# Optimization experiments

Measured on AMD Instinct MI355X. Metric: run time of the kernel, lower is better.

The kernel has to match this reference:

```python
import jax, jax.numpy as jnp
import numpy as np

B, T, D, H, F = 4, 2048, 1024, 16, 4096
HD = D // H
EPS = 1e-5


def setup_inputs() -> dict:
    key = jax.random.key(0)
    ks = jax.random.split(key, 10)
    s = lambda fan_in: 1.0 / np.sqrt(fan_in)
    return {
        "x": jax.random.normal(ks[0], (B, T, D), jnp.float32),
        "ln1_g": jnp.ones((D,), jnp.float32),
        "ln1_b": jnp.zeros((D,), jnp.float32),
        "ln2_g": jnp.ones((D,), jnp.float32),
        "ln2_b": jnp.zeros((D,), jnp.float32),
        "Wq": jax.random.normal(ks[1], (H, D, HD), jnp.float32) * s(D),
        "Wk": jax.random.normal(ks[2], (H, D, HD), jnp.float32) * s(D),
        "Wv": jax.random.normal(ks[3], (H, D, HD), jnp.float32) * s(D),
        "Wo": jax.random.normal(ks[4], (D, D), jnp.float32) * s(D),
        "bo": jnp.zeros((D,), jnp.float32),
        "W1": jax.random.normal(ks[5], (D, F), jnp.float32) * s(D),
        "b1": jnp.zeros((F,), jnp.float32),
        "W2": jax.random.normal(ks[6], (F, D), jnp.float32) * s(F),
        "b2": jnp.zeros((D,), jnp.float32),
    }


def _layernorm(x, g, b):
    mu = jnp.mean(x, axis=-1, keepdims=True)
    var = jnp.mean(jnp.square(x - mu), axis=-1, keepdims=True)
    return (x - mu) * jax.lax.rsqrt(var + EPS) * g + b


def reference(x, ln1_g, ln1_b, ln2_g, ln2_b, Wq, Wk, Wv, Wo, bo, W1, b1, W2, b2):
    Bc, Tc, Dc = x.shape
    xn = _layernorm(x, ln1_g, ln1_b)
    # per-head projections (source loops over heads; here batched over h)
    q = jnp.einsum('btd,hdk->bhtk', xn, Wq)
    k = jnp.einsum('btd,hdk->bhtk', xn, Wk)
    v = jnp.einsum('btd,hdk->bhtk', xn, Wv)
    scale = jnp.asarray(Dc, x.dtype) ** -0.5  # C**-0.5 with C = embedding_dim
    scores = jnp.einsum('bhtk,bhsk->bhts', q, k) * scale
    causal = jnp.tril(jnp.ones((Tc, Tc), bool))
    scores = jnp.where(causal, scores, -jnp.inf)
    attn = jax.nn.softmax(scores, axis=-1)
    out = jnp.einsum('bhts,bhsk->bhtk', attn, v)
    out = out.transpose(0, 2, 1, 3).reshape(Bc, Tc, Dc)  # concat heads
    attn_out = out @ Wo + bo
    h = attn_out + x  # residual 1
    hn = _layernorm(h, ln2_g, ln2_b)
    ff = jax.nn.relu(hn @ W1 + b1) @ W2 + b2
    return ff + h  # residual 2
```

## Files before the change

kernel.cpp:

```cpp
#include <hip/hip_runtime.h>
#include <hip/hip_bf16.h>

#define NB 4
#define NT 2048
#define ND 1024
#define NH 16
#define NHD 64
#define NF 4096
#define MTOK (NB*NT)

typedef float f32x4 __attribute__((ext_vector_type(4)));
typedef __bf16 bf16x8 __attribute__((ext_vector_type(8)));
typedef short s16x8 __attribute__((ext_vector_type(8)));
typedef unsigned short ushort_t;

__device__ inline ushort_t f2bf(float f) {
    unsigned int u = __builtin_bit_cast(unsigned int, f);
    unsigned int r = (u + 0x7FFFu + ((u >> 16) & 1u)) >> 16;
    return (ushort_t)r;
}
__device__ inline float bf2f(ushort_t u) {
    return __builtin_bit_cast(float, (unsigned int)u << 16);
}

__device__ __forceinline__ void async_load16(const void* g, void* l) {
    __builtin_amdgcn_global_load_lds(
        (const __attribute__((address_space(1))) void*)g,
        (__attribute__((address_space(3))) void*)l, 16, 0, 0);
}

__device__ __forceinline__ unsigned int cvt_pk_bf16(float lo, float hi) {
    unsigned int r;
    asm("v_cvt_pk_bf16_f32 %0, %1, %2" : "=v"(r) : "v"(lo), "v"(hi));
    return r;
}

__device__ __forceinline__ float exp2_fast(float x) {
    float r;
    asm("v_exp_f32 %0, %1" : "=v"(r) : "v"(x));
    return r;
}

__global__ __launch_bounds__(256)
void transpose_to_bf16(const float* __restrict__ src, ushort_t* __restrict__ dst,
                       int R, int C) {
    __shared__ float tile[32][33];
    int c0 = blockIdx.x * 32, r0 = blockIdx.y * 32;
    #pragma unroll
    for (int i = 0; i < 32; i += 8)
        tile[threadIdx.y + i][threadIdx.x] =
            src[(size_t)(r0 + threadIdx.y + i) * C + c0 + threadIdx.x];
    __syncthreads();
    #pragma unroll
    for (int i = 0; i < 32; i += 8)
        dst[(size_t)(c0 + threadIdx.y + i) * R + r0 + threadIdx.x] =
            f2bf(tile[threadIdx.x][threadIdx.y + i]);
}

__global__ __launch_bounds__(256)
void transpose_qkv_to_bf16(const float* __restrict__ Wq, const float* __restrict__ Wk,
                           const float* __restrict__ Wv, ushort_t* __restrict__ dst) {
    __shared__ float tile[32][33];
    int z = blockIdx.z;
    int w = z >> 4, h = z & 15;
    const float* src = (w == 0 ? Wq : (w == 1 ? Wk : Wv)) + (size_t)h * ND * NHD;
    const float sc = (w == 0) ? 0.03125f * 1.44269504f : 1.0f;
    ushort_t* out = dst + ((size_t)w * ND + h * NHD) * ND;
    int c0 = blockIdx.x * 32, r0 = blockIdx.y * 32;
    #pragma unroll
    for (int i = 0; i < 32; i += 8)
        tile[threadIdx.y + i][threadIdx.x] =
            src[(size_t)(r0 + threadIdx.y + i) * NHD + c0 + threadIdx.x];
    __syncthreads();
    #pragma unroll
    for (int i = 0; i < 32; i += 8)
        out[(size_t)(c0 + threadIdx.y + i) * ND + r0 + threadIdx.x] =
            f2bf(tile[threadIdx.x][threadIdx.y + i] * sc);
}

__global__ __launch_bounds__(256)
void layernorm_to_bf16(const float* __restrict__ x, const float* __restrict__ g,
                       const float* __restrict__ bvec, ushort_t* __restrict__ out) {
    int row = blockIdx.x;
    const float4* xr = (const float4*)(x + (size_t)row * ND);
    float4 v = xr[threadIdx.x];
    float s = v.x + v.y + v.z + v.w;
    float s2 = v.x * v.x + v.y * v.y + v.z * v.z + v.w * v.w;
    #pragma unroll
    for (int o = 32; o >= 1; o >>= 1) {
        s += __shfl_xor(s, o);
        s2 += __shfl_xor(s2, o);
    }
    __shared__ float red[8];
    int wave = threadIdx.x >> 6, lane = threadIdx.x & 63;
    if (lane == 0) { red[wave] = s; red[4 + wave] = s2; }
    __syncthreads();
    float ts = red[0] + red[1] + red[2] + red[3];
    float ts2 = red[4] + red[5] + red[6] + red[7];
    float mu = ts * (1.f / ND);
    float var = ts2 * (1.f / ND) - mu * mu;
    float rs = rsqrtf(var + 1e-5f);
    float4 gv = ((const float4*)g)[threadIdx.x];
    float4 bv = ((const float4*)bvec)[threadIdx.x];
    ushort4 o4;
    o4.x = f2bf((v.x - mu) * rs * gv.x + bv.x);
    o4.y = f2bf((v.y - mu) * rs * gv.y + bv.y);
    o4.z = f2bf((v.z - mu) * rs * gv.z + bv.z);
    o4.w = f2bf((v.w - mu) * rs * gv.w + bv.w);
    ((ushort4*)(out + (size_t)row * ND))[threadIdx.x] = o4;
}

__global__ __launch_bounds__(256)
void layernorm_bf16(const ushort_t* __restrict__ x, const float* __restrict__ g,
                    const float* __restrict__ bvec, ushort_t* __restrict__ out) {
    int row = blockIdx.x;
    ushort4 u4 = ((const ushort4*)(x + (size_t)row * ND))[threadIdx.x];
    float4 v;
    v.x = bf2f(u4.x); v.y = bf2f(u4.y); v.z = bf2f(u4.z); v.w = bf2f(u4.w);
    float s = v.x + v.y + v.z + v.w;
    float s2 = v.x * v.x + v.y * v.y + v.z * v.z + v.w * v.w;
    #pragma unroll
    for (int o = 32; o >= 1; o >>= 1) {
        s += __shfl_xor(s, o);
        s2 += __shfl_xor(s2, o);
    }
    __shared__ float red[8];
    int wave = threadIdx.x >> 6, lane = threadIdx.x & 63;
    if (lane == 0) { red[wave] = s; red[4 + wave] = s2; }
    __syncthreads();
    float ts = red[0] + red[1] + red[2] + red[3];
    float ts2 = red[4] + red[5] + red[6] + red[7];
    float mu = ts * (1.f / ND);
    float var = ts2 * (1.f / ND) - mu * mu;
    float rs = rsqrtf(var + 1e-5f);
    float4 gv = ((const float4*)g)[threadIdx.x];
    float4 bv = ((const float4*)bvec)[threadIdx.x];
    ushort4 o4;
    o4.x = f2bf((v.x - mu) * rs * gv.x + bv.x);
    o4.y = f2bf((v.y - mu) * rs * gv.y + bv.y);
    o4.z = f2bf((v.z - mu) * rs * gv.z + bv.z);
    o4.w = f2bf((v.w - mu) * rs * gv.w + bv.w);
    ((ushort4*)(out + (size_t)row * ND))[threadIdx.x] = o4;
}

template<int BN, bool HAS_BIAS, bool RELU, int RES_MODE, bool OUT_F32>
__global__ __launch_bounds__(512, 2)
void gemm8p(const ushort_t* __restrict__ A, const ushort_t* __restrict__ Bt,
            const float* __restrict__ bias, const void* __restrict__ res,
            void* __restrict__ outp, int M, int N, int K) {
    constexpr int NFR = BN / 64;
    __shared__ __align__(16) ushort_t As[2][256 * 64];
    __shared__ __align__(16) ushort_t Bs[2][BN * 64];
    const int t = threadIdx.x;
    const int wave = t >> 6, lane = t & 63;
    const int wm = wave >> 2, wn = wave & 3;
    const int g = lane >> 4, l16 = lane & 15;
    int wid = blockIdx.y * gridDim.x + blockIdx.x;
    const int cpx = (gridDim.x * gridDim.y) >> 3;
    wid = (wid & 7) * cpx + (wid >> 3);
    const int m0 = (wid / gridDim.x) * 256;
    const int n0 = (wid % gridDim.x) * BN;
    const int lrow8 = lane >> 3;
    const int srcCol = ((lane & 7) ^ lrow8) * 8;
    const ushort_t* Abase = A + (size_t)m0 * K + srcCol;
    const ushort_t* Bbase = Bt + (size_t)n0 * K + srcCol;
    const int NKT = K >> 6;

    f32x4 acc[8][NFR] = {};

    auto stageAhalf = [&](int kt, int h, int slot) {
        #pragma unroll
        for (int j = 2 * h; j < 2 * h + 2; j++) {
            const int rowbase = j * 64 + wave * 8;
            async_load16(Abase + (size_t)(rowbase + lrow8) * K + kt * 64,
                         &As[slot][rowbase * 64]);
        }
    };
    auto stageBhalf = [&](int kt, int h, int slot) {
        if constexpr (BN == 256) {
            #pragma unroll
            for (int j = 2 * h; j < 2 * h + 2; j++) {
                const int rowbase = j * 64 + wave * 8;
                async_load16(Bbase + (size_t)(rowbase + lrow8) * K + kt * 64,
                             &Bs[slot][rowbase * 64]);
            }
        } else {
            const int rowbase = h * 64 + wave * 8;
            async_load16(Bbase + (size_t)(rowbase + lrow8) * K + kt * 64,
                         &Bs[slot][rowbase * 64]);
        }
    };

    stageAhalf(0, 0, 0); stageAhalf(0, 1, 0);
    stageBhalf(0, 0, 0); stageBhalf(0, 1, 0);
    stageBhalf(1, 0, 1); stageBhalf(1, 1, 1);
    stageAhalf(1, 0, 1);
    if constexpr (BN == 256) asm volatile("s_waitcnt vmcnt(6)" ::: "memory");
    else                     asm volatile("s_waitcnt vmcnt(4)" ::: "memory");
    __builtin_amdgcn_s_barrier();
    __builtin_amdgcn_sched_barrier(0);

    for (int kt = 0; kt < NKT; ++kt) {
        const int cur = kt & 1, nxt = cur ^ 1;
        const ushort_t* as = As[cur];
        const ushort_t* bs = Bs[cur];
        bf16x8 bfr[NFR][2];

        if constexpr (BN == 128) {
            #pragma unroll
            for (int ph = 0; ph < 2; ph++) {
                if (ph == 0) {
                    #pragma unroll
                    for (int nf = 0; nf < NFR; nf++)
                        #pragma unroll
                        for (int ks = 0; ks < 2; ks++) {
                            const int row = wn * (BN / 4) + nf * 16 + l16;
                            int a = row * 128 + ks * 64 + 16 * g;
                            a ^= (row & 7) << 4;
                            bfr[nf][ks] = *(const bf16x8*)((const char*)bs + a);
                        }
                }
                bf16x8 af[2][2][2];
                #pragma unroll
                for (int qq = 0; qq < 2; qq++)
                    #pragma unroll
                    for (int mi2 = 0; mi2 < 2; mi2++)
                        #pragma unroll
                        for (int ks = 0; ks < 2; ks++) {
                            const int row = (ph * 2 + qq) * 64 + wm * 32 + mi2 * 16 + l16;
                            int a = row * 128 + ks * 64 + 16 * g;
                            a ^= (row & 7) << 4;
                            af[qq][mi2][ks] = *(const bf16x8*)((const char*)as + a);
                        }
                if (ph == 0) {
                    if (kt + 1 < NKT) stageAhalf(kt + 1, 1, nxt);
                } else {
                    if (kt + 2 < NKT) {
                        stageBhalf(kt + 2, 0, cur);
                        stageBhalf(kt + 2, 1, cur);
                        stageAhalf(kt + 2, 0, cur);
                    }
                }
                __builtin_amdgcn_sched_barrier(0);
                if (ph == 1) {
                    if (kt >= NKT - 2) asm volatile("s_waitcnt vmcnt(0)" ::: "memory");
                    else               asm volatile("s_waitcnt vmcnt(4)" ::: "memory");
                }
                __builtin_amdgcn_s_barrier();
                __builtin_amdgcn_sched_barrier(0);
                __builtin_amdgcn_s_setprio(1);
                #pragma unroll
                for (int qq = 0; qq < 2; qq++)
                    #pragma unroll
                    for (int mi2 = 0; mi2 < 2; mi2++)
                        #pragma unroll
                        for (int nf = 0; nf < NFR; nf++)
                            #pragma unroll
                            for (int ks = 0; ks < 2; ks++)
                                acc[(ph * 2 + qq) * 2 + mi2][nf] =
                                    __builtin_amdgcn_mfma_f32_16x16x32_bf16(
                                        af[qq][mi2][ks], bfr[nf][ks],
                                        acc[(ph * 2 + qq) * 2 + mi2][nf], 0, 0, 0);
                __builtin_amdgcn_s_setprio(0);
                __builtin_amdgcn_s_barrier();
                __builtin_amdgcn_sched_barrier(0);
            }
        } else {
            #pragma unroll
            for (int q = 0; q < 4; q++) {
                if (q == 0) {
                    #pragma unroll
                    for (int nf = 0; nf < NFR; nf++)
                        #pragma unroll
                        for (int ks = 0; ks < 2; ks++) {
                            const int row = wn * (BN / 4) + nf * 16 + l16;
                            int a = row * 128 + ks * 64 + 16 * g;
                            a ^= (row & 7) << 4;
                            bfr[nf][ks] = *(const bf16x8*)((const char*)bs + a);
                        }
                }
                bf16x8 af[2][2];
                #pragma unroll
                for (int mi2 = 0; mi2 < 2; mi2++)
                    #pragma unroll
                    for (int ks = 0; ks < 2; ks++) {
                        const int row = q * 64 + wm * 32 + mi2 * 16 + l16;
                        int a = row * 128 + ks * 64 + 16 * g;
                        a ^= (row & 7) << 4;
                        af[mi2][ks] = *(const bf16x8*)((const char*)as + a);
                    }
                if (q == 0)      { if (kt + 1 < NKT) stageAhalf(kt + 1, 1, nxt); }
                else if (q == 1) { if (kt + 2 < NKT) stageBhalf(kt + 2, 0, cur); }
                else if (q == 2) { if (kt + 2 < NKT) stageBhalf(kt + 2, 1, cur); }
                else             { if (kt + 2 < NKT) stageAhalf(kt + 2, 0, cur); }
                __builtin_amdgcn_sched_barrier(0);
                if (q == 3) {
                    if (kt >= NKT - 2) asm volatile("s_waitcnt vmcnt(0)" ::: "memory");
                    else               asm volatile("s_waitcnt vmcnt(6)" ::: "memory");
                }
                __builtin_amdgcn_s_barrier();
                __builtin_amdgcn_sched_barrier(0);
                __builtin_amdgcn_s_setprio(1);
                #pragma unroll
                for (int mi2 = 0; mi2 < 2; mi2++)
                    #pragma unroll
                    for (int nf = 0; nf < NFR; nf++)
                        #pragma unroll
                        for (int ks = 0; ks < 2; ks++)
                            acc[q * 2 + mi2][nf] = __builtin_amdgcn_mfma_f32_16x16x32_bf16(
                                af[mi2][ks], bfr[nf][ks], acc[q * 2 + mi2][nf], 0, 0, 0);
                __builtin_amdgcn_s_setprio(0);
                __builtin_amdgcn_s_barrier();
                __builtin_amdgcn_sched_barrier(0);
            }
        }
    }

    const int gc0 = n0 + wn * (BN / 4) + l16;
    #pragma unroll
    for (int mi = 0; mi < 8; mi++) {
        const int rowb = m0 + (mi >> 1) * 64 + wm * 32 + (mi & 1) * 16 + g * 4;
        #pragma unroll
        for (int nf = 0; nf < NFR; nf++) {
            const int col = gc0 + nf * 16;
            float bb = 0.f;
            if constexpr (HAS_BIAS) bb = bias[col];
            #pragma unroll
            for (int r = 0; r < 4; r++) {
                const int row = rowb + r;
                float v = acc[mi][nf][r] + bb;
                if constexpr (RELU) v = fmaxf(v, 0.f);
                if constexpr (RES_MODE == 1)
                    v += ((const float*)res)[(size_t)row * N + col];
                else if constexpr (RES_MODE == 2)
                    v += bf2f(((const ushort_t*)res)[(size_t)row * N + col]);
                if constexpr (OUT_F32)
                    ((float*)outp)[(size_t)row * N + col] = v;
                else
                    ((ushort_t*)outp)[(size_t)row * N + col] = f2bf(v);
            }
        }
    }
}

__global__ __launch_bounds__(256)
void attn_kernel(const ushort_t* __restrict__ qkv, ushort_t* __restrict__ out) {
    __shared__ __align__(16) ushort_t Ks[2][64 * 64];
    __shared__ __align__(16) ushort_t Vt[2][64 * 64];
    __shared__ unsigned int Pw[4][32][35];
    const int L = blockIdx.y * gridDim.x + blockIdx.x;
    const int xcd = L & 7, kk = L >> 3;
    const int bh = ((kk & 7) << 3) | xcd;
    const int pairIdx = kk >> 3;
    const int b = bh >> 4, h = bh & 15;
    const int t = threadIdx.x, wave = t >> 6, lane = t & 63;
    const int g = lane >> 4, q16 = lane & 15;
    const size_t base = ((size_t)b * NT) * 3072 + h * NHD;
    const ushort_t* qp_base = qkv + base;
    const ushort_t* kb = qkv + base + 1024;
    const ushort_t* vb = qkv + base + 2048;
    const int krw = lane >> 3, kck = lane & 7;
    const int ksrc = (kck ^ krw) * 8;
    const int vkp = t >> 3, vdg = t & 7;

    bf16x8 ones_f;
    {
        uint4 u = {0x3F803F80u, 0x3F803F80u, 0x3F803F80u, 0x3F803F80u};
        ones_f = __builtin_bit_cast(bf16x8, u);
    }

    auto stageK = [&](int kv, int buf) {
        #pragma unroll
        for (int c = 0; c < 2; c++) {
            const int rowbase = c * 32 + wave * 8;
            async_load16(kb + (size_t)(kv * 64 + rowbase + krw) * 3072 + ksrc,
                         &Ks[buf][rowbase * 64]);
        }
    };
    auto loadV = [&](int kv, s16x8& v0, s16x8& v1) {
        const ushort_t* vp = vb + (size_t)(kv * 64 + 2 * vkp) * 3072 + vdg * 8;
        v0 = *(const s16x8*)vp;
        v1 = *(const s16x8*)(vp + 3072);
    };
    auto writeV = [&](int buf, const s16x8& v0, const s16x8& v1) {
        const uint4 w0 = __builtin_bit_cast(uint4, v0);
        const uint4 w1 = __builtin_bit_cast(uint4, v1);
        const unsigned int lw0[4] = {w0.x, w0.y, w0.z, w0.w};
        const unsigned int lw1[4] = {w1.x, w1.y, w1.z, w1.w};
        #pragma unroll
        for (int j = 0; j < 4; j++) {
            unsigned int we = __builtin_amdgcn_perm(lw1[j], lw0[j], 0x05040100u);
            unsigned int wo = __builtin_amdgcn_perm(lw1[j], lw0[j], 0x07060302u);
            int d0 = vdg * 8 + 2 * j;
            int a0 = (d0 << 7) + (vkp << 2);
            a0 ^= ((((d0) & 7) ^ (((d0) >> 3) & 7)) << 4);
            *(unsigned int*)((char*)&Vt[buf][0] + a0) = we;
            int d1 = d0 + 1;
            int a1 = (d1 << 7) + (vkp << 2);
            a1 ^= ((((d1) & 7) ^ (((d1) >> 3) & 7)) << 4);
            *(unsigned int*)((char*)&Vt[buf][0] + a1) = wo;
        }
    };

    for (int half = 0; half < 2; half++) {
        const int qt = half ? (15 - pairIdx) : pairIdx;
        const int q0 = qt * 128;
        const int wq0 = q0 + wave * 32;
        bf16x8 qf[2][2];
        #pragma unroll
        for (int qb2 = 0; qb2 < 2; qb2++) {
            const ushort_t* qp = qp_base + (size_t)(wq0 + 16 * qb2 + q16) * 3072 + 8 * g;
            qf[qb2][0] = *(const bf16x8*)qp;
            qf[qb2][1] = *(const bf16x8*)(qp + 32);
        }
        f32x4 of[2][4] = {};
        f32x4 of4[2] = {};
        const int nkv = 2 * qt + 2;

        {
            s16x8 pv0, pv1;
            stageK(0, 0);
            loadV(0, pv0, pv1);
            asm volatile("s_waitcnt vmcnt(0)" ::: "memory");
            writeV(0, pv0, pv1);
        }
        __syncthreads();

        for (int kv = 0; kv < nkv; ++kv) {
            const int cur = kv & 1, nxt = cur ^ 1;
            s16x8 pv0, pv1;
            const bool pre = (kv + 1 < nkv);
            if (pre) {
                stageK(kv + 1, nxt);
                loadV(kv + 1, pv0, pv1);
            }
            __builtin_amdgcn_sched_barrier(0);

            const int kbase = kv * 64;
            if (kbase <= wq0 + 31) {
                bf16x8 kf[4][2];
                #pragma unroll
                for (int n = 0; n < 4; n++)
                    #pragma unroll
                    for (int kd = 0; kd < 2; kd++) {
                        int row = n * 16 + q16;
                        int a = row * 128 + (kd * 64 + 16 * g);
                        a ^= ((row & 7) << 4);
                        kf[n][kd] = *(const bf16x8*)((const char*)&Ks[cur][0] + a);
                    }

                f32x4 sf[2][4] = {};
                #pragma unroll
                for (int n = 0; n < 4; n++)
                    #pragma unroll
                    for (int kd = 0; kd < 2; kd++) {
                        sf[0][n] = __builtin_amdgcn_mfma_f32_16x16x32_bf16(
                            kf[n][kd], qf[0][kd], sf[0][n], 0, 0, 0);
                        sf[1][n] = __builtin_amdgcn_mfma_f32_16x16x32_bf16(
                            kf[n][kd], qf[1][kd], sf[1][n], 0, 0, 0);
                    }

                #pragma unroll
                for (int qb2 = 0; qb2 < 2; qb2++) {
                    const int wqb = wq0 + 16 * qb2 + q16;
                    const bool partial = (kbase + 63 > wq0 + 16 * qb2);
                    float p[4][4];
                    #pragma unroll
                    for (int n = 0; n < 4; n++)
                        #pragma unroll
                        for (int r = 0; r < 4; r++) {
                            float v = sf[qb2][n][r];
                            if (partial) {
                                int kg = kbase + n * 16 + 4 * g + r;
                                if (kg > wqb) v = -1.0e30f;
                            }
                            p[n][r] = exp2_fast(v);
                        }
                    unsigned int* pr = &Pw[wave][16 * qb2 + q16][0];
                    #pragma unroll
                    for (int n = 0; n < 4; n++) {
                        pr[8 * n + 2 * g + 0] = cvt_pk_bf16(p[n][0], p[n][1]);
                        pr[8 * n + 2 * g + 1] = cvt_pk_bf16(p[n][2], p[n][3]);
                    }
                }

                #pragma unroll
                for (int kbk = 0; kbk < 2; kbk++) {
                    bf16x8 pfr[2];
                    #pragma unroll
                    for (int qb2 = 0; qb2 < 2; qb2++) {
                        const unsigned int* pr = &Pw[wave][16 * qb2 + q16][0];
                        uint4 pu;
                        pu.x = pr[16 * kbk + 4 * g + 0];
                        pu.y = pr[16 * kbk + 4 * g + 1];
                        pu.z = pr[16 * kbk + 4 * g + 2];
                        pu.w = pr[16 * kbk + 4 * g + 3];
                        pfr[qb2] = __builtin_bit_cast(bf16x8, pu);
                    }
                    of4[0] = __builtin_amdgcn_mfma_f32_16x16x32_bf16(
                        ones_f, pfr[0], of4[0], 0, 0, 0);
                    of4[1] = __builtin_amdgcn_mfma_f32_16x16x32_bf16(
                        ones_f, pfr[1], of4[1], 0, 0, 0);
                    #pragma unroll
                    for (int nf = 0; nf < 4; nf++) {
                        const int d = nf * 16 + q16;
                        int a = (d << 7) + (kbk * 64 + 16 * g);
                        a ^= (((d & 7) ^ ((d >> 3) & 7)) << 4);
                        bf16x8 vf = *(const bf16x8*)((const char*)&Vt[cur][0] + a);
                        of[0][nf] = __builtin_amdgcn_mfma_f32_16x16x32_bf16(
                            vf, pfr[0], of[0][nf], 0, 0, 0);
                        of[1][nf] = __builtin_amdgcn_mfma_f32_16x16x32_bf16(
                            vf, pfr[1], of[1][nf], 0, 0, 0);
                    }
                }
            }

            if (pre) writeV(nxt, pv0, pv1);
            __syncthreads();
        }

        #pragma unroll
        for (int qb2 = 0; qb2 < 2; qb2++) {
            float rl = 1.f / of4[qb2][0];
            const size_t orow = (size_t)b * NT + q0 + wave * 32 + 16 * qb2 + q16;
            #pragma unroll
            for (int nf = 0; nf < 4; nf++) {
                ushort4 o4;
                o4.x = f2bf(of[qb2][nf][0] * rl);
                o4.y = f2bf(of[qb2][nf][1] * rl);
                o4.z = f2bf(of[qb2][nf][2] * rl);
                o4.w = f2bf(of[qb2][nf][3] * rl);
                *(ushort4*)(out + orow * ND + h * NHD + nf * 16 + 4 * g) = o4;
            }
        }
    }
}

extern "C" void kernel_launch(void* const* d_in, const int* in_sizes, int n_in,
                              void* d_out, int out_size, void* d_ws, size_t ws_size,
                              hipStream_t stream) {
    const float* x     = (const float*)d_in[0];
    const float* ln1_g = (const float*)d_in[1];
    const float* ln1_b = (const float*)d_in[2];
    const float* ln2_g = (const float*)d_in[3];
    const float* ln2_b = (const float*)d_in[4];
    const float* Wq    = (const float*)d_in[5];
    const float* Wk    = (const float*)d_in[6];
    const float* Wv    = (const float*)d_in[7];
    const float* Wo    = (const float*)d_in[8];
    const float* bo    = (const float*)d_in[9];
    const float* W1    = (const float*)d_in[10];
    const float* b1    = (const float*)d_in[11];
    const float* W2    = (const float*)d_in[12];
    const float* b2    = (const float*)d_in[13];
    float* outp = (float*)d_out;

    char* w = (char*)d_ws;
    ushort_t* Wqkv_t = (ushort_t*)(w);
    ushort_t* Wo_t   = (ushort_t*)(w + 6291456);
    ushort_t* W1_t   = (ushort_t*)(w + 8388608);
    ushort_t* W2_t   = (ushort_t*)(w + 16777216);
    ushort_t* xn     = (ushort_t*)(w + 25165824);
    ushort_t* qkv    = (ushort_t*)(w + 41943040);
    ushort_t* attn_o = qkv + (size_t)MTOK * 3072;
    ushort_t* ff1    = qkv;
    ushort_t* hbuf   = (ushort_t*)(w + 41943040 + 67108864);

    dim3 tb(32, 8);
    transpose_qkv_to_bf16<<<dim3(2, 32, 48), tb, 0, stream>>>(Wq, Wk, Wv, Wqkv_t);
    transpose_to_bf16<<<dim3(32, 32), tb, 0, stream>>>(Wo, Wo_t, 1024, 1024);
    transpose_to_bf16<<<dim3(128, 32), tb, 0, stream>>>(W1, W1_t, 1024, 4096);
    transpose_to_bf16<<<dim3(32, 128), tb, 0, stream>>>(W2, W2_t, 4096, 1024);

    layernorm_to_bf16<<<MTOK, 256, 0, stream>>>(x, ln1_g, ln1_b, xn);

    gemm8p<128, false, false, 0, false><<<dim3(24, 32), 512, 0, stream>>>(
        xn, Wqkv_t, nullptr, nullptr, qkv, MTOK, 3072, 1024);

    attn_kernel<<<dim3(8, 64), 256, 0, stream>>>(qkv, attn_o);

    gemm8p<128, true, false, 1, false><<<dim3(8, 32), 512, 0, stream>>>(
        attn_o, Wo_t, bo, x, hbuf, MTOK, 1024, 1024);

    layernorm_bf16<<<MTOK, 256, 0, stream>>>(hbuf, ln2_g, ln2_b, xn);

    gemm8p<256, true, true, 0, false><<<dim3(16, 32), 512, 0, stream>>>(
        xn, W1_t, b1, nullptr, ff1, MTOK, NF, 1024);

    gemm8p<128, true, false, 2, true><<<dim3(8, 32), 512, 0, stream>>>(
        ff1, W2_t, b2, hbuf, outp, MTOK, 1024, NF);
}
```

Baseline: 357.3 us.

## Use 128x128-tile two-buffer GEMM kernel for the W2 projection

```diff
diff --git a/kernel.cpp b/kernel.cpp
--- a/kernel.cpp
+++ b/kernel.cpp
@@ -343,6 +343,118 @@
     }
 }
 
+template<bool HAS_BIAS, bool RELU, int RES_MODE, bool OUT_F32>
+__global__ __launch_bounds__(256, 2)
+void gemm2b64(const ushort_t* __restrict__ A, const ushort_t* __restrict__ Bt,
+              const float* __restrict__ bias, const void* __restrict__ res,
+              void* __restrict__ outp, int M, int N, int K) {
+    __shared__ __align__(16) ushort_t As[2][128 * 64];
+    __shared__ __align__(16) ushort_t Bs[2][128 * 64];
+    const int t = threadIdx.x;
+    const int wave = t >> 6, lane = t & 63;
+    const int wm = wave >> 1, wn = wave & 1;
+    const int g = lane >> 4, l16 = lane & 15;
+    int wid = blockIdx.y * gridDim.x + blockIdx.x;
+    const int cpx = (gridDim.x * gridDim.y) >> 3;
+    wid = (wid & 7) * cpx + (wid >> 3);
+    const int m0 = (wid / gridDim.x) * 128;
+    const int n0 = (wid % gridDim.x) * 128;
+    const int rw = lane >> 3, ck = lane & 7;
+    const int srcCol = (ck ^ rw) * 8;
+    const ushort_t* Abase = A + (size_t)m0 * K + srcCol;
+    const ushort_t* Bbase = Bt + (size_t)n0 * K + srcCol;
+    const int NKT = K >> 6;
+
+    f32x4 acc[4][4] = {};
+
+    auto stage = [&](int kt, int slot) {
+        #pragma unroll
+        for (int j = 0; j < 4; j++) {
+            const int rowbase = j * 32 + wave * 8;
+            async_load16(Abase + (size_t)(rowbase + rw) * K + kt * 64,
+                         &As[slot][rowbase * 64]);
+        }
+        #pragma unroll
+        for (int j = 0; j < 4; j++) {
+            const int rowbase = j * 32 + wave * 8;
+            async_load16(Bbase + (size_t)(rowbase + rw) * K + kt * 64,
+                         &Bs[slot][rowbase * 64]);
+        }
+    };
+
+    stage(0, 0);
+    stage(1, 1);
+
+    for (int kt = 0; kt < NKT; ++kt) {
+        const int cur = kt & 1;
+        if (kt >= NKT - 1) asm volatile("s_waitcnt vmcnt(0)" ::: "memory");
+        else               asm volatile("s_waitcnt vmcnt(8)" ::: "memory");
+        __builtin_amdgcn_s_barrier();
+        __builtin_amdgcn_sched_barrier(0);
+
+        const ushort_t* as = As[cur];
+        const ushort_t* bs = Bs[cur];
+        bf16x8 af[4][2], bfr[4][2];
+        #pragma unroll
+        for (int mi = 0; mi < 4; mi++)
+            #pragma unroll
+            for (int ks = 0; ks < 2; ks++) {
+                const int row = wm * 64 + mi * 16 + l16;
+                int a = row * 128 + ks * 64 + 16 * g;
+                a ^= (row & 7) << 4;
+                af[mi][ks] = *(const bf16x8*)((const char*)as + a);
+            }
+        #pragma unroll
+        for (int nf = 0; nf < 4; nf++)
+            #pragma unroll
+            for (int ks = 0; ks < 2; ks++) {
+                const int row = wn * 64 + nf * 16 + l16;
+                int a = row * 128 + ks * 64 + 16 * g;
+                a ^= (row & 7) << 4;
+                bfr[nf][ks] = *(const bf16x8*)((const char*)bs + a);
+            }
+        __builtin_amdgcn_s_setprio(1);
+        #pragma unroll
+        for (int mi = 0; mi < 4; mi++)
+            #pragma unroll
+            for (int nf = 0; nf < 4; nf++)
+                #pragma unroll
+                for (int ks = 0; ks < 2; ks++)
+                    acc[mi][nf] = __builtin_amdgcn_mfma_f32_16x16x32_bf16(
+                        af[mi][ks], bfr[nf][ks], acc[mi][nf], 0, 0, 0);
+        __builtin_amdgcn_s_setprio(0);
+        __builtin_amdgcn_s_barrier();
+        __builtin_amdgcn_sched_barrier(0);
+        if (kt + 2 < NKT) stage(kt + 2, cur);
+    }
+
+    const int gc0 = n0 + wn * 64 + l16;
+    #pragma unroll
+    for (int mi = 0; mi < 4; mi++) {
+        const int rowb = m0 + wm * 64 + mi * 16 + g * 4;
+        #pragma unroll
+        for (int nf = 0; nf < 4; nf++) {
+            const int col = gc0 + nf * 16;
+            float bb = 0.f;
+            if constexpr (HAS_BIAS) bb = bias[col];
+            #pragma unroll
+            for (int r = 0; r < 4; r++) {
+                const int row = rowb + r;
+                float v = acc[mi][nf][r] + bb;
+                if constexpr (RELU) v = fmaxf(v, 0.f);
+                if constexpr (RES_MODE == 1)
+                    v += ((const float*)res)[(size_t)row * N + col];
+                else if constexpr (RES_MODE == 2)
+                    v += bf2f(((const ushort_t*)res)[(size_t)row * N + col]);
+                if constexpr (OUT_F32)
+                    ((float*)outp)[(size_t)row * N + col] = v;
+                else
+                    ((ushort_t*)outp)[(size_t)row * N + col] = f2bf(v);
+            }
+        }
+    }
+}
+
 __global__ __launch_bounds__(256)
 void attn_kernel(const ushort_t* __restrict__ qkv, ushort_t* __restrict__ out) {
     __shared__ __align__(16) ushort_t Ks[2][64 * 64];
@@ -587,6 +699,6 @@
     gemm8p<256, true, true, 0, false><<<dim3(16, 32), 512, 0, stream>>>(
         xn, W1_t, b1, nullptr, ff1, MTOK, NF, 1024);
 
-    gemm8p<128, true, false, 2, true><<<dim3(8, 32), 512, 0, stream>>>(
+    gemm2b64<true, false, 2, true><<<dim3(8, 64), 256, 0, stream>>>(
         ff1, W2_t, b2, hbuf, outp, MTOK, 1024, NF);
 }
```

Result: no change. 352.5 us (-1.3%).
